# Performance work log

Hardware: AMD Instinct MI355X
Metric: run time of the kernel (lower is better)

Reference implementation:

```python
import jax, jax.numpy as jnp
import numpy as np

V = 50257      # vocab_size
EMB = 300      # emb_size
H = 512        # mcan_flat_out_size (GRU hidden)
HS = 256       # hidden_size (object proposal feature dim)
BH = 256       # bi_hidden_size (encoder output feature dim)
NP = 256       # num_proposal
ML = 50        # max_length (lang seq len)
AL = 20        # answer length -> 19 decode steps
NEG = -1e9


def setup_inputs() -> dict:
    key = jax.random.key(0)
    ks = jax.random.split(key, 30)
    s = 0.02
    n = lambda k, sh: (s * jax.random.normal(k, sh)).astype(jnp.float32)
    d = {}
    d["input_tok"] = jax.random.randint(ks[0], (1,), 0, V, dtype=jnp.int32)
    d["hidden"] = jax.random.normal(ks[1], (1, 1, H), jnp.float32)
    d["encoder_outputs"] = jax.random.normal(ks[2], (ML, BH), jnp.float32)
    d["object_proposals"] = jax.random.normal(ks[3], (NP, HS), jnp.float32)
    d["object_mask"] = jax.random.randint(ks[4], (1, NP), 0, 2, dtype=jnp.int32)
    d["lang_mask"] = jax.random.randint(ks[5], (1, ML), 0, 2, dtype=jnp.int32)
    d["answer_to_vocab"] = jax.random.randint(ks[6], (AL,), 0, V, dtype=jnp.int32)
    # learned params (dropout treated as eval/identity)
    d["emb"] = n(ks[7], (V, EMB))
    cin = H + EMB  # 812
    d["attn_w1"] = n(ks[8], (256, cin)); d["attn_b1"] = jnp.zeros((256,), jnp.float32)
    d["attn_w2"] = n(ks[9], (ML, 256)); d["attn_b2"] = jnp.zeros((ML,), jnp.float32)
    d["attn_op_w1"] = n(ks[10], (256, cin)); d["attn_op_b1"] = jnp.zeros((256,), jnp.float32)
    d["attn_op_w2"] = n(ks[11], (NP, 256)); d["attn_op_b2"] = jnp.zeros((NP,), jnp.float32)
    comb_in = HS + BH + EMB  # 812
    d["cmb_w1"] = n(ks[12], (512, comb_in)); d["cmb_b1"] = jnp.zeros((512,), jnp.float32)
    d["cmb_w2"] = n(ks[13], (H, 512)); d["cmb_b2"] = jnp.zeros((H,), jnp.float32)
    d["gru_w_ih"] = n(ks[14], (3 * H, H)); d["gru_w_hh"] = n(ks[15], (3 * H, H))
    d["gru_b_ih"] = jnp.zeros((3 * H,), jnp.float32); d["gru_b_hh"] = jnp.zeros((3 * H,), jnp.float32)
    d["out_w"] = n(ks[16], (V, H)); d["out_b"] = jnp.zeros((V,), jnp.float32)
    return d


def reference(input_tok, hidden, encoder_outputs, object_proposals, object_mask,
              lang_mask, answer_to_vocab, emb, attn_w1, attn_b1, attn_w2, attn_b2,
              attn_op_w1, attn_op_b1, attn_op_w2, attn_op_b2, cmb_w1, cmb_b1,
              cmb_w2, cmb_b2, gru_w_ih, gru_w_hh, gru_b_ih, gru_b_hh, out_w, out_b):
    obj_m = object_mask.astype(bool)   # [1, NP]
    lang_m = lang_mask.astype(bool)    # [1, ML]
    # teacher forcing: step i embeds answer_to_vocab[i] (step 0 uses input_tok)
    tokens = jnp.concatenate([input_tok, answer_to_vocab[1:-1]])  # [AL-1]

    def step(h, tok):
        # h: [1,1,H]
        x = jax.nn.relu(emb[tok])[None, :]                     # [1,EMB]
        cat = jnp.concatenate([x, h[0]], axis=1)               # [1, EMB+H]
        # object attention
        a_op = jax.nn.relu(cat @ attn_op_w1.T + attn_op_b1) @ attn_op_w2.T + attn_op_b2
        a_op = jax.nn.softmax(jnp.where(obj_m, NEG, a_op), axis=1)   # [1,NP]
        ctx_op = a_op @ object_proposals                       # [1,HS]
        # language attention
        a_l = jax.nn.relu(cat @ attn_w1.T + attn_b1) @ attn_w2.T + attn_b2
        a_l = jax.nn.softmax(jnp.where(lang_m, NEG, a_l), axis=1)    # [1,ML]
        ctx = a_l @ encoder_outputs                            # [1,BH]
        comb = jnp.concatenate([x, ctx, ctx_op], axis=1)       # [1, EMB+BH+HS]
        g = jax.nn.relu(jax.nn.relu(comb @ cmb_w1.T + cmb_b1) @ cmb_w2.T + cmb_b2)  # [1,H]
        # GRU cell (torch gate order: r, z, n)
        gi = g @ gru_w_ih.T + gru_b_ih
        gh = h[0] @ gru_w_hh.T + gru_b_hh
        i_r, i_z, i_n = jnp.split(gi, 3, axis=1)
        h_r, h_z, h_n = jnp.split(gh, 3, axis=1)
        r = jax.nn.sigmoid(i_r + h_r)
        z = jax.nn.sigmoid(i_z + h_z)
        nn_ = jnp.tanh(i_n + r * h_n)
        h_new = (1.0 - z) * nn_ + z * h[0]                     # [1,H]
        logits = h_new @ out_w.T + out_b                       # [1,V]
        return h_new[None], (logits, a_l, a_op)

    _, (logits, attn_w, attn_ob_w) = jax.lax.scan(step, hidden, tokens)
    # logits: [AL-1,1,V]; attn_w: [AL-1,1,ML]; attn_ob_w: [AL-1,1,NP]
    return logits, attn_w, attn_ob_w
```

## Files before the change

### kernel.cpp

```cpp
#include <hip/hip_runtime.h>
#include <math.h>

#define T_STEPS 19
#define V 50257
#define EMB 300
#define HDIM 512
#define NP 256
#define ML 50
#define CIN 812
#define NEGV -1e9f
#define NBLK 64

#define OFF_X      0
#define OFF_POP    5700
#define OFF_PL     10564
#define OFF_PC     15428
#define OFF_HS     25156
#define OFF_H1OP   35396
#define OFF_H1L    35652
#define OFF_C1     37444
#define OFF_G      37956
#define OFF_LOGOP  38468
#define OFF_LOGL   38724
#define OFF_MPROP  38788
#define OFF_MENC   169860
#define OFF_BAR    195460

#define OUT_LOGITS 0
#define OUT_ATTW   ((long)T_STEPS * V)
#define OUT_ATTOB  (OUT_ATTW + (long)T_STEPS * ML)

__device__ __forceinline__ float wred(float v) {
  v += __shfl_xor(v, 32, 64);
  v += __shfl_xor(v, 16, 64);
  v += __shfl_xor(v, 8, 64);
  v += __shfl_xor(v, 4, 64);
  v += __shfl_xor(v, 2, 64);
  v += __shfl_xor(v, 1, 64);
  return v;
}

__device__ __forceinline__ float dot4(float4 a, float4 b) {
  return a.x * b.x + a.y * b.y + a.z * b.z + a.w * b.w;
}

__device__ __forceinline__ void gstore(float* p, float v) {
  __hip_atomic_store(p, v, __ATOMIC_RELAXED, __HIP_MEMORY_SCOPE_AGENT);
}
__device__ __forceinline__ float ld1c(const float* p) {
  return __hip_atomic_load(p, __ATOMIC_RELAXED, __HIP_MEMORY_SCOPE_AGENT);
}
__device__ __forceinline__ float2 ld2c(const float* p) {
  unsigned long long u = __hip_atomic_load((const unsigned long long*)p,
                                           __ATOMIC_RELAXED, __HIP_MEMORY_SCOPE_AGENT);
  float2 r;
  r.x = __uint_as_float((unsigned)u);
  r.y = __uint_as_float((unsigned)(u >> 32));
  return r;
}
__device__ __forceinline__ float4 ld4c(const float* p) {
  float2 a = ld2c(p), b = ld2c(p + 2);
  return make_float4(a.x, a.y, b.x, b.y);
}

__device__ __forceinline__ void gbar(float* wsb, unsigned bar) {
  asm volatile("s_waitcnt vmcnt(0)" ::: "memory");
  __syncthreads();
  unsigned* flags = (unsigned*)(wsb + OFF_BAR) + 16;
  if (threadIdx.x == 0) {
    __hip_atomic_store(flags + 16 * blockIdx.x, bar, __ATOMIC_RELAXED, __HIP_MEMORY_SCOPE_AGENT);
  }
  asm volatile("" ::: "memory");
  if (threadIdx.x < 64) {
    unsigned* f = flags + 16 * threadIdx.x;
    while (__hip_atomic_load(f, __ATOMIC_RELAXED, __HIP_MEMORY_SCOPE_AGENT) < bar) {
      __builtin_amdgcn_s_sleep(1);
    }
  }
  __syncthreads();
}

__global__ void k_pre1(const int* __restrict__ tok0, const int* __restrict__ ans,
                       const float* __restrict__ emb, const float* __restrict__ hidden,
                       float* __restrict__ ws) {
  int tid = blockIdx.x * 256 + threadIdx.x;
  if (tid < T_STEPS * EMB) {
    int s = tid / EMB, j = tid - s * EMB;
    int t = (s == 0) ? tok0[0] : ans[s];
    float v = emb[(long)t * EMB + j];
    ws[OFF_X + tid] = v > 0.f ? v : 0.f;
  } else {
    int k = tid - T_STEPS * EMB;
    if (k < HDIM) ws[OFF_HS + k] = hidden[k];
  }
}

__global__ void k_pre2(const float* __restrict__ w1op, const float* __restrict__ b1op,
                       const float* __restrict__ w1l,  const float* __restrict__ b1l,
                       const float* __restrict__ wc1,  const float* __restrict__ bc1,
                       float* __restrict__ ws) {
  int gw = (blockIdx.x * 256 + threadIdx.x) >> 6;
  int lane = threadIdx.x & 63;
  int s = gw >> 10;
  int rr = gw & 1023;
  if (s >= T_STEPS) return;
  const float* wrow; const float* bias; float* dst; int r;
  if (rr < 256)      { r = rr;       wrow = w1op + (long)r * CIN; bias = b1op; dst = ws + OFF_POP + s * 256 + r; }
  else if (rr < 512) { r = rr - 256; wrow = w1l  + (long)r * CIN; bias = b1l;  dst = ws + OFF_PL  + s * 256 + r; }
  else               { r = rr - 512; wrow = wc1  + (long)r * CIN; bias = bc1;  dst = ws + OFF_PC  + s * 512 + r; }
  const float* x = ws + OFF_X + s * EMB;
  float acc = 0.f;
#pragma unroll
  for (int it = 0; it < 5; ++it) {
    int j = it * 64 + lane;
    if (j < EMB) acc += wrow[j] * x[j];
  }
  acc = wred(acc);
  if (lane == 0) *dst = acc + bias[r];
}

#define LDSF 12850
__global__ void __launch_bounds__(256) k_mprep(const float* __restrict__ cw1,
                                               const float* __restrict__ prop,
                                               const float* __restrict__ enc,
                                               float* __restrict__ ws) {
  __shared__ float lds[LDSF];
  int tid = threadIdx.x, r = blockIdx.x;
  float acc = 0.f;
  for (int kc = 0; kc < 8; ++kc) {
    __syncthreads();
#pragma unroll
    for (int i = 0; i < 8; ++i) {
      int f = tid + 256 * i; int row = f >> 3, q = f & 7;
      float4 v = *(const float4*)(prop + (long)row * 256 + kc * 32 + 4 * q);
      float* p = lds + row * 33 + 4 * q;
      p[0] = v.x; p[1] = v.y; p[2] = v.z; p[3] = v.w;
    }
    __syncthreads();
    const float* wbase = cw1 + (long)r * CIN + 556 + kc * 32;
    const float* pl = lds + tid * 33;
#pragma unroll
    for (int k4 = 0; k4 < 8; ++k4) {
      float4 w4 = *(const float4*)(wbase + 4 * k4);
      const float* pp = pl + 4 * k4;
      acc += w4.x * pp[0] + w4.y * pp[1] + w4.z * pp[2] + w4.w * pp[3];
    }
  }
  ws[OFF_MPROP + (long)r * 256 + tid] = acc;
  __syncthreads();
  for (int i = 0; i < 13; ++i) {
    int f = tid + 256 * i;
    if (f < 3200) {
      int row = f >> 6, q = f & 63;
      float4 v = *(const float4*)(enc + (long)row * 256 + 4 * q);
      float* p = lds + row * 257 + 4 * q;
      p[0] = v.x; p[1] = v.y; p[2] = v.z; p[3] = v.w;
    }
  }
  __syncthreads();
  if (tid < ML) {
    const float* wb2 = cw1 + (long)r * CIN + 300;
    const float* el = lds + tid * 257;
    float a2 = 0.f;
#pragma unroll 8
    for (int k = 0; k < 256; ++k) a2 += wb2[k] * el[k];
    ws[OFF_MENC + (long)r * ML + tid] = a2;
  }
}

__global__ void __launch_bounds__(256) k_recur(
    const float* __restrict__ w1op, const float* __restrict__ w1l,
    const float* __restrict__ whh,  const float* __restrict__ bhh,
    const float* __restrict__ w2op, const float* __restrict__ b2op,
    const float* __restrict__ w2l,  const float* __restrict__ b2l,
    const int* __restrict__ obj_mask, const int* __restrict__ lang_mask,
    const float* __restrict__ wc2,  const float* __restrict__ bc2,
    const float* __restrict__ wih,  const float* __restrict__ bih,
    float* ws, float* __restrict__ out) {
  const int tid = threadIdx.x;
  const int lane = tid & 63;
  const int wv = (blockIdx.x << 2) + (tid >> 6);
  const int r0 = 2 * wv, r1 = 2 * wv + 1;
  unsigned bar = 1;
  __shared__ float red[256];
  __shared__ __align__(16) float sm_aop[256];
  __shared__ float sm_al[64];

  for (int s = 0; s < T_STEPS; ++s) {
    float ghr0, ghz0, ghn0, ghr1, ghz1, ghn1;
    {
      const float* h = ws + OFF_HS + s * HDIM;
      float4 ha = ld4c(h + 4 * lane);
      float4 hb = ld4c(h + 256 + 4 * lane);
      const float* wa0 = (r0 < 256) ? (w1op + (long)r0 * CIN + 300) : (w1l + (long)(r0 - 256) * CIN + 300);
      const float* wa1 = (r1 < 256) ? (w1op + (long)r1 * CIN + 300) : (w1l + (long)(r1 - 256) * CIN + 300);
      float a0 = dot4(*(const float4*)(wa0 + 4 * lane), ha) + dot4(*(const float4*)(wa0 + 256 + 4 * lane), hb);
      float a1 = dot4(*(const float4*)(wa1 + 4 * lane), ha) + dot4(*(const float4*)(wa1 + 256 + 4 * lane), hb);
      const float* p0 = whh + (long)r0 * HDIM;
      const float* p1 = whh + (long)(r0 + 512) * HDIM;
      const float* p2 = whh + (long)(r0 + 1024) * HDIM;
      const float* p3 = whh + (long)r1 * HDIM;
      const float* p4 = whh + (long)(r1 + 512) * HDIM;
      const float* p5 = whh + (long)(r1 + 1024) * HDIM;
      float b0 = dot4(*(const float4*)(p0 + 4 * lane), ha) + dot4(*(const float4*)(p0 + 256 + 4 * lane), hb);
      float b1 = dot4(*(const float4*)(p1 + 4 * lane), ha) + dot4(*(const float4*)(p1 + 256 + 4 * lane), hb);
      float b2 = dot4(*(const float4*)(p2 + 4 * lane), ha) + dot4(*(const float4*)(p2 + 256 + 4 * lane), hb);
      float b3 = dot4(*(const float4*)(p3 + 4 * lane), ha) + dot4(*(const float4*)(p3 + 256 + 4 * lane), hb);
      float b4 = dot4(*(const float4*)(p4 + 4 * lane), ha) + dot4(*(const float4*)(p4 + 256 + 4 * lane), hb);
      float b5 = dot4(*(const float4*)(p5 + 4 * lane), ha) + dot4(*(const float4*)(p5 + 256 + 4 * lane), hb);
      a0 = wred(a0); a1 = wred(a1);
      b0 = wred(b0); b1 = wred(b1); b2 = wred(b2);
      b3 = wred(b3); b4 = wred(b4); b5 = wred(b5);
      ghr0 = b0 + bhh[r0]; ghz0 = b1 + bhh[512 + r0]; ghn0 = b2 + bhh[1024 + r0];
      ghr1 = b3 + bhh[r1]; ghz1 = b4 + bhh[512 + r1]; ghn1 = b5 + bhh[1024 + r1];
      if (lane == 0) {
        float v0 = a0 + ((r0 < 256) ? ws[OFF_POP + s * 256 + r0] : ws[OFF_PL + s * 256 + (r0 - 256)]);
        float v1 = a1 + ((r1 < 256) ? ws[OFF_POP + s * 256 + r1] : ws[OFF_PL + s * 256 + (r1 - 256)]);
        float* d0 = (r0 < 256) ? (ws + OFF_H1OP + r0) : (ws + OFF_H1L + (r0 - 256));
        float* d1 = (r1 < 256) ? (ws + OFF_H1OP + r1) : (ws + OFF_H1L + (r1 - 256));
        gstore(d0, v0 > 0.f ? v0 : 0.f);
        gstore(d1, v1 > 0.f ? v1 : 0.f);
      }
    }
    gbar(ws, bar++);
    {
      float4 h1 = ld4c(ws + OFF_H1OP + 4 * lane);
      const float* wr = w2op + (long)wv * 256;
      float acc = wred(dot4(*(const float4*)(wr + 4 * lane), h1));
      if (lane == 0) gstore(ws + OFF_LOGOP + wv, acc + b2op[wv]);
      if (wv < ML) {
        float4 h1l = ld4c(ws + OFF_H1L + 4 * lane);
        const float* wrl = w2l + (long)wv * 256;
        float accl = wred(dot4(*(const float4*)(wrl + 4 * lane), h1l));
        if (lane == 0) gstore(ws + OFF_LOGL + wv, accl + b2l[wv]);
      }
    }
    gbar(ws, bar++);
    {
      float lv = ld1c(ws + OFF_LOGOP + tid);
      float vo = (obj_mask[tid] != 0) ? NEGV : lv;
      red[tid] = vo; __syncthreads();
      for (int st = 128; st > 0; st >>= 1) { if (tid < st) red[tid] = fmaxf(red[tid], red[tid + st]); __syncthreads(); }
      float mo = red[0]; __syncthreads();
      float eo = expf(vo - mo);
      red[tid] = eo; __syncthreads();
      for (int st = 128; st > 0; st >>= 1) { if (tid < st) red[tid] += red[tid + st]; __syncthreads(); }
      float aop = eo / red[0];
      sm_aop[tid] = aop;
      __syncthreads();
      float ll = (tid < ML) ? ld1c(ws + OFF_LOGL + tid) : 0.f;
      float vl = (tid < ML) ? ((lang_mask[tid] != 0) ? NEGV : ll) : -3e38f;
      red[tid] = vl; __syncthreads();
      for (int st = 128; st > 0; st >>= 1) { if (tid < st) red[tid] = fmaxf(red[tid], red[tid + st]); __syncthreads(); }
      float ml_ = red[0]; __syncthreads();
      float el = (tid < ML) ? expf(vl - ml_) : 0.f;
      red[tid] = el; __syncthreads();
      for (int st = 128; st > 0; st >>= 1) { if (tid < st) red[tid] += red[tid + st]; __syncthreads(); }
      float al = el / red[0];
      if (tid < 64) sm_al[tid] = (tid < ML) ? al : 0.f;
      __syncthreads();
      if (blockIdx.x == 0) {
        out[OUT_ATTOB + (long)s * NP + tid] = aop;
        if (tid < ML) out[OUT_ATTW + (long)s * ML + tid] = al;
      }
      float4 a4 = *(const float4*)(&sm_aop[4 * lane]);
      const float* mp0 = ws + OFF_MPROP + (long)r0 * 256;
      const float* mp1 = ws + OFF_MPROP + (long)r1 * 256;
      float acc0 = dot4(*(const float4*)(mp0 + 4 * lane), a4);
      float acc1 = dot4(*(const float4*)(mp1 + 4 * lane), a4);
      if (lane < ML) {
        float alv = sm_al[lane];
        acc0 += ws[OFF_MENC + (long)r0 * ML + lane] * alv;
        acc1 += ws[OFF_MENC + (long)r1 * ML + lane] * alv;
      }
      acc0 = wred(acc0); acc1 = wred(acc1);
      if (lane == 0) {
        float v0 = acc0 + ws[OFF_PC + s * HDIM + r0];
        float v1 = acc1 + ws[OFF_PC + s * HDIM + r1];
        gstore(ws + OFF_C1 + r0, v0 > 0.f ? v0 : 0.f);
        gstore(ws + OFF_C1 + r1, v1 > 0.f ? v1 : 0.f);
      }
    }
    gbar(ws, bar++);
    {
      float4 ca = ld4c(ws + OFF_C1 + 4 * lane);
      float4 cb = ld4c(ws + OFF_C1 + 256 + 4 * lane);
      const float* q0 = wc2 + (long)r0 * HDIM;
      const float* q1 = wc2 + (long)r1 * HDIM;
      float acc0 = dot4(*(const float4*)(q0 + 4 * lane), ca) + dot4(*(const float4*)(q0 + 256 + 4 * lane), cb);
      float acc1 = dot4(*(const float4*)(q1 + 4 * lane), ca) + dot4(*(const float4*)(q1 + 256 + 4 * lane), cb);
      acc0 = wred(acc0); acc1 = wred(acc1);
      if (lane == 0) {
        float v0 = acc0 + bc2[r0];
        float v1 = acc1 + bc2[r1];
        gstore(ws + OFF_G + r0, v0 > 0.f ? v0 : 0.f);
        gstore(ws + OFF_G + r1, v1 > 0.f ? v1 : 0.f);
      }
    }
    gbar(ws, bar++);
    {
      float4 ga = ld4c(ws + OFF_G + 4 * lane);
      float4 gb = ld4c(ws + OFF_G + 256 + 4 * lane);
      const float* p0 = wih + (long)r0 * HDIM;
      const float* p1 = wih + (long)(r0 + 512) * HDIM;
      const float* p2 = wih + (long)(r0 + 1024) * HDIM;
      const float* p3 = wih + (long)r1 * HDIM;
      const float* p4 = wih + (long)(r1 + 512) * HDIM;
      const float* p5 = wih + (long)(r1 + 1024) * HDIM;
      float a0 = dot4(*(const float4*)(p0 + 4 * lane), ga) + dot4(*(const float4*)(p0 + 256 + 4 * lane), gb);
      float a1 = dot4(*(const float4*)(p1 + 4 * lane), ga) + dot4(*(const float4*)(p1 + 256 + 4 * lane), gb);
      float a2 = dot4(*(const float4*)(p2 + 4 * lane), ga) + dot4(*(const float4*)(p2 + 256 + 4 * lane), gb);
      float a3 = dot4(*(const float4*)(p3 + 4 * lane), ga) + dot4(*(const float4*)(p3 + 256 + 4 * lane), gb);
      float a4_ = dot4(*(const float4*)(p4 + 4 * lane), ga) + dot4(*(const float4*)(p4 + 256 + 4 * lane), gb);
      float a5 = dot4(*(const float4*)(p5 + 4 * lane), ga) + dot4(*(const float4*)(p5 + 256 + 4 * lane), gb);
      a0 = wred(a0); a1 = wred(a1); a2 = wred(a2);
      a3 = wred(a3); a4_ = wred(a4_); a5 = wred(a5);
      if (lane == 0) {
        float ir0 = a0 + bih[r0], iz0 = a1 + bih[512 + r0], in0 = a2 + bih[1024 + r0];
        float rg0 = 1.f / (1.f + expf(-(ir0 + ghr0)));
        float zg0 = 1.f / (1.f + expf(-(iz0 + ghz0)));
        float ng0 = tanhf(in0 + rg0 * ghn0);
        float hp0 = ld1c(ws + OFF_HS + s * HDIM + r0);
        gstore(ws + OFF_HS + (s + 1) * HDIM + r0, (1.f - zg0) * ng0 + zg0 * hp0);
        float ir1 = a3 + bih[r1], iz1 = a4_ + bih[512 + r1], in1 = a5 + bih[1024 + r1];
        float rg1 = 1.f / (1.f + expf(-(ir1 + ghr1)));
        float zg1 = 1.f / (1.f + expf(-(iz1 + ghz1)));
        float ng1 = tanhf(in1 + rg1 * ghn1);
        float hp1 = ld1c(ws + OFF_HS + s * HDIM + r1);
        gstore(ws + OFF_HS + (s + 1) * HDIM + r1, (1.f - zg1) * ng1 + zg1 * hp1);
      }
    }
    gbar(ws, bar++);
  }
}

__global__ void __launch_bounds__(256) k_final2(const float* __restrict__ ow,
                                                const float* __restrict__ ob,
                                                const float* __restrict__ ws,
                                                float* __restrict__ out) {
  __shared__ __align__(16) float wl[256 * 36];
  __shared__ __align__(16) float hl[T_STEPS * 512];
  int tid = threadIdx.x;
  long rbase = (long)blockIdx.x * 256;
  for (int i = tid; i < T_STEPS * 512; i += 256) hl[i] = ws[OFF_HS + 512 + i];
  float4 st[8];
#pragma unroll
  for (int i = 0; i < 8; ++i) {
    int f = tid + 256 * i; int row = f >> 3, q = f & 7;
    long r = rbase + row;
    st[i] = (r < V) ? *(const float4*)(ow + r * 512 + 4 * q) : make_float4(0.f, 0.f, 0.f, 0.f);
  }
  float acc[T_STEPS];
#pragma unroll
  for (int s = 0; s < T_STEPS; ++s) acc[s] = 0.f;
  __syncthreads();
  for (int c = 0; c < 16; ++c) {
#pragma unroll
    for (int i = 0; i < 8; ++i) {
      int f = tid + 256 * i; int row = f >> 3, q = f & 7;
      float* p = wl + row * 36 + 4 * q;
      p[0] = st[i].x; p[1] = st[i].y; p[2] = st[i].z; p[3] = st[i].w;
    }
    __syncthreads();
    if (c < 15) {
#pragma unroll
      for (int i = 0; i < 8; ++i) {
        int f = tid + 256 * i; int row = f >> 3, q = f & 7;
        long r = rbase + row;
        st[i] = (r < V) ? *(const float4*)(ow + r * 512 + (c + 1) * 32 + 4 * q) : make_float4(0.f, 0.f, 0.f, 0.f);
      }
    }
    const float* wp = wl + tid * 36;
#pragma unroll
    for (int kq = 0; kq < 8; ++kq) {
      float4 w4 = *(const float4*)(wp + 4 * kq);
      const float* hb = hl + c * 32 + 4 * kq;
#pragma unroll
      for (int s = 0; s < T_STEPS; ++s) {
        float4 h4 = *(const float4*)(hb + s * 512);
        acc[s] += dot4(w4, h4);
      }
    }
    __syncthreads();
  }
  long r = rbase + tid;
  if (r < V) {
    float b = ob[r];
#pragma unroll
    for (int s = 0; s < T_STEPS; ++s) out[OUT_LOGITS + (long)s * V + r] = acc[s] + b;
  }
}

extern "C" void kernel_launch(void* const* d_in, const int* in_sizes, int n_in,
                              void* d_out, int out_size, void* d_ws, size_t ws_size,
                              hipStream_t stream) {
  const int*   input_tok  = (const int*)d_in[0];
  const float* hidden     = (const float*)d_in[1];
  const float* enc        = (const float*)d_in[2];
  const float* prop       = (const float*)d_in[3];
  const int*   obj_mask   = (const int*)d_in[4];
  const int*   lang_mask  = (const int*)d_in[5];
  const int*   ans        = (const int*)d_in[6];
  const float* emb        = (const float*)d_in[7];
  const float* attn_w1    = (const float*)d_in[8];
  const float* attn_b1    = (const float*)d_in[9];
  const float* attn_w2    = (const float*)d_in[10];
  const float* attn_b2    = (const float*)d_in[11];
  const float* attn_op_w1 = (const float*)d_in[12];
  const float* attn_op_b1 = (const float*)d_in[13];
  const float* attn_op_w2 = (const float*)d_in[14];
  const float* attn_op_b2 = (const float*)d_in[15];
  const float* cmb_w1     = (const float*)d_in[16];
  const float* cmb_b1     = (const float*)d_in[17];
  const float* cmb_w2     = (const float*)d_in[18];
  const float* cmb_b2     = (const float*)d_in[19];
  const float* gw_ih      = (const float*)d_in[20];
  const float* gw_hh      = (const float*)d_in[21];
  const float* gb_ih      = (const float*)d_in[22];
  const float* gb_hh      = (const float*)d_in[23];
  const float* out_w      = (const float*)d_in[24];
  const float* out_b      = (const float*)d_in[25];
  float* out = (float*)d_out;
  float* ws  = (float*)d_ws;

  hipMemsetAsync((char*)d_ws + (size_t)OFF_BAR * 4, 0, 8448, stream);
  k_pre1<<<25, 256, 0, stream>>>(input_tok, ans, emb, hidden, ws);
  k_pre2<<<4864, 256, 0, stream>>>(attn_op_w1, attn_op_b1, attn_w1, attn_b1, cmb_w1, cmb_b1, ws);
  k_mprep<<<512, 256, 0, stream>>>(cmb_w1, prop, enc, ws);
  k_recur<<<NBLK, 256, 0, stream>>>(attn_op_w1, attn_w1, gw_hh, gb_hh,
                                    attn_op_w2, attn_op_b2, attn_w2, attn_b2,
                                    obj_mask, lang_mask, cmb_w2, cmb_b2,
                                    gw_ih, gb_ih, ws, out);
  k_final2<<<(V + 255) / 256, 256, 0, stream>>>(out_w, out_b, ws, out);
}
```

Baseline: 419.2 us.

## Keep recurrent weights in registers across steps and transpose final LDS tile

The persistent recurrent kernel now loads every weight slice it needs (attention W1 hidden part, GRU W_hh/W_ih, combine W2, attention W2, precomputed proposal and encoder projections, biases) into registers once before the step loop, instead of re-reading them from global memory or cache in each of the 19 steps. It sets launch bounds to one block per CU to allow the higher register count. The output-projection kernel changes its LDS weight tile to a transposed layout with float4 stores, to cut bank conflicts and scalar stores. Workspace offsets and the barrier memset size are also compacted.

```diff
diff --git a/kernel.cpp b/kernel.cpp
--- a/kernel.cpp
+++ b/kernel.cpp
@@ -18,13 +18,13 @@
 #define OFF_HS     25156
 #define OFF_H1OP   35396
 #define OFF_H1L    35652
-#define OFF_C1     37444
-#define OFF_G      37956
-#define OFF_LOGOP  38468
-#define OFF_LOGL   38724
-#define OFF_MPROP  38788
-#define OFF_MENC   169860
-#define OFF_BAR    195460
+#define OFF_C1     35908
+#define OFF_G      36420
+#define OFF_LOGOP  36932
+#define OFF_LOGL   37188
+#define OFF_MPROP  37252
+#define OFF_MENC   168324
+#define OFF_BAR    193924
 
 #define OUT_LOGITS 0
 #define OUT_ATTW   ((long)T_STEPS * V)
@@ -168,7 +168,7 @@
   }
 }
 
-__global__ void __launch_bounds__(256) k_recur(
+__global__ void __launch_bounds__(256, 1) k_recur(
     const float* __restrict__ w1op, const float* __restrict__ w1l,
     const float* __restrict__ whh,  const float* __restrict__ bhh,
     const float* __restrict__ w2op, const float* __restrict__ b2op,
@@ -181,38 +181,64 @@
   const int lane = tid & 63;
   const int wv = (blockIdx.x << 2) + (tid >> 6);
   const int r0 = 2 * wv, r1 = 2 * wv + 1;
+  const int l4 = 4 * lane;
   unsigned bar = 1;
   __shared__ float red[256];
   __shared__ __align__(16) float sm_aop[256];
   __shared__ float sm_al[64];
 
+  const float* wa0p = (r0 < 256) ? (w1op + (long)r0 * CIN + 300) : (w1l + (long)(r0 - 256) * CIN + 300);
+  const float* wa1p = (r1 < 256) ? (w1op + (long)r1 * CIN + 300) : (w1l + (long)(r1 - 256) * CIN + 300);
+  float4 WA00 = *(const float4*)(wa0p + l4), WA01 = *(const float4*)(wa0p + 256 + l4);
+  float4 WA10 = *(const float4*)(wa1p + l4), WA11 = *(const float4*)(wa1p + 256 + l4);
+  const float* q;
+  q = whh + (long)r0 * HDIM;           float4 WH00 = *(const float4*)(q + l4), WH01 = *(const float4*)(q + 256 + l4);
+  q = whh + (long)(r0 + 512) * HDIM;   float4 WH10 = *(const float4*)(q + l4), WH11 = *(const float4*)(q + 256 + l4);
+  q = whh + (long)(r0 + 1024) * HDIM;  float4 WH20 = *(const float4*)(q + l4), WH21 = *(const float4*)(q + 256 + l4);
+  q = whh + (long)r1 * HDIM;           float4 WH30 = *(const float4*)(q + l4), WH31 = *(const float4*)(q + 256 + l4);
+  q = whh + (long)(r1 + 512) * HDIM;   float4 WH40 = *(const float4*)(q + l4), WH41 = *(const float4*)(q + 256 + l4);
+  q = whh + (long)(r1 + 1024) * HDIM;  float4 WH50 = *(const float4*)(q + l4), WH51 = *(const float4*)(q + 256 + l4);
+  float4 W2  = *(const float4*)(w2op + (long)wv * 256 + l4);
+  float4 W2L = (wv < ML) ? *(const float4*)(w2l + (long)wv * 256 + l4) : make_float4(0.f, 0.f, 0.f, 0.f);
+  float4 MP0 = *(const float4*)(ws + OFF_MPROP + (long)r0 * 256 + l4);
+  float4 MP1 = *(const float4*)(ws + OFF_MPROP + (long)r1 * 256 + l4);
+  float  ME0 = (lane < ML) ? ws[OFF_MENC + (long)r0 * ML + lane] : 0.f;
+  float  ME1 = (lane < ML) ? ws[OFF_MENC + (long)r1 * ML + lane] : 0.f;
+  q = wc2 + (long)r0 * HDIM;           float4 WC00 = *(const float4*)(q + l4), WC01 = *(const float4*)(q + 256 + l4);
+  q = wc2 + (long)r1 * HDIM;           float4 WC10 = *(const float4*)(q + l4), WC11 = *(const float4*)(q + 256 + l4);
+  q = wih + (long)r0 * HDIM;           float4 WI00 = *(const float4*)(q + l4), WI01 = *(const float4*)(q + 256 + l4);
+  q = wih + (long)(r0 + 512) * HDIM;   float4 WI10 = *(const float4*)(q + l4), WI11 = *(const float4*)(q + 256 + l4);
+  q = wih + (long)(r0 + 1024) * HDIM;  float4 WI20 = *(const float4*)(q + l4), WI21 = *(const float4*)(q + 256 + l4);
+  q = wih + (long)r1 * HDIM;           float4 WI30 = *(const float4*)(q + l4), WI31 = *(const float4*)(q + 256 + l4);
+  q = wih + (long)(r1 + 512) * HDIM;   float4 WI40 = *(const float4*)(q + l4), WI41 = *(const float4*)(q + 256 + l4);
+  q = wih + (long)(r1 + 1024) * HDIM;  float4 WI50 = *(const float4*)(q + l4), WI51 = *(const float4*)(q + 256 + l4);
+  float BH0 = bhh[r0], BH1 = bhh[512 + r0], BH2 = bhh[1024 + r0];
+  float BH3 = bhh[r1], BH4 = bhh[512 + r1], BH5 = bhh[1024 + r1];
+  float BI0 = bih[r0], BI1 = bih[512 + r0], BI2 = bih[1024 + r0];
+  float BI3 = bih[r1], BI4 = bih[512 + r1], BI5 = bih[1024 + r1];
+  float BC0 = bc2[r0], BC1 = bc2[r1];
+  float B2  = b2op[wv];
+  float B2Lv = (wv < ML) ? b2l[wv] : 0.f;
+
   for (int s = 0; s < T_STEPS; ++s) {
     float ghr0, ghz0, ghn0, ghr1, ghz1, ghn1;
     {
       const float* h = ws + OFF_HS + s * HDIM;
-      float4 ha = ld4c(h + 4 * lane);
-      float4 hb = ld4c(h + 256 + 4 * lane);
-      const float* wa0 = (r0 < 256) ? (w1op + (long)r0 * CIN + 300) : (w1l + (long)(r0 - 256) * CIN + 300);
-      const float* wa1 = (r1 < 256) ? (w1op + (long)r1 * CIN + 300) : (w1l + (long)(r1 - 256) * CIN + 300);
-      float a0 = dot4(*(const float4*)(wa0 + 4 * lane), ha) + dot4(*(const float4*)(wa0 + 256 + 4 * lane), hb);
-      float a1 = dot4(*(const float4*)(wa1 + 4 * lane), ha) + dot4(*(const float4*)(wa1 + 256 + 4 * lane), hb);
-      const float* p0 = whh + (long)r0 * HDIM;
-      const float* p1 = whh + (long)(r0 + 512) * HDIM;
-      const float* p2 = whh + (long)(r0 + 1024) * HDIM;
-      const float* p3 = whh + (long)r1 * HDIM;
-      const float* p4 = whh + (long)(r1 + 512) * HDIM;
-      const float* p5 = whh + (long)(r1 + 1024) * HDIM;
-      float b0 = dot4(*(const float4*)(p0 + 4 * lane), ha) + dot4(*(const float4*)(p0 + 256 + 4 * lane), hb);
-      float b1 = dot4(*(const float4*)(p1 + 4 * lane), ha) + dot4(*(const float4*)(p1 + 256 + 4 * lane), hb);
-      float b2 = dot4(*(const float4*)(p2 + 4 * lane), ha) + dot4(*(const float4*)(p2 + 256 + 4 * lane), hb);
-      float b3 = dot4(*(const float4*)(p3 + 4 * lane), ha) + dot4(*(const float4*)(p3 + 256 + 4 * lane), hb);
-      float b4 = dot4(*(const float4*)(p4 + 4 * lane), ha) + dot4(*(const float4*)(p4 + 256 + 4 * lane), hb);
-      float b5 = dot4(*(const float4*)(p5 + 4 * lane), ha) + dot4(*(const float4*)(p5 + 256 + 4 * lane), hb);
+      float4 ha = ld4c(h + l4);
+      float4 hb = ld4c(h + 256 + l4);
+      float a0 = dot4(WA00, ha) + dot4(WA01, hb);
+      float a1 = dot4(WA10, ha) + dot4(WA11, hb);
+      float b0 = dot4(WH00, ha) + dot4(WH01, hb);
+      float b1 = dot4(WH10, ha) + dot4(WH11, hb);
+      float b2 = dot4(WH20, ha) + dot4(WH21, hb);
+      float b3 = dot4(WH30, ha) + dot4(WH31, hb);
+      float b4 = dot4(WH40, ha) + dot4(WH41, hb);
+      float b5 = dot4(WH50, ha) + dot4(WH51, hb);
       a0 = wred(a0); a1 = wred(a1);
       b0 = wred(b0); b1 = wred(b1); b2 = wred(b2);
       b3 = wred(b3); b4 = wred(b4); b5 = wred(b5);
-      ghr0 = b0 + bhh[r0]; ghz0 = b1 + bhh[512 + r0]; ghn0 = b2 + bhh[1024 + r0];
-      ghr1 = b3 + bhh[r1]; ghz1 = b4 + bhh[512 + r1]; ghn1 = b5 + bhh[1024 + r1];
+      ghr0 = b0 + BH0; ghz0 = b1 + BH1; ghn0 = b2 + BH2;
+      ghr1 = b3 + BH3; ghz1 = b4 + BH4; ghn1 = b5 + BH5;
       if (lane == 0) {
         float v0 = a0 + ((r0 < 256) ? ws[OFF_POP + s * 256 + r0] : ws[OFF_PL + s * 256 + (r0 - 256)]);
         float v1 = a1 + ((r1 < 256) ? ws[OFF_POP + s * 256 + r1] : ws[OFF_PL + s * 256 + (r1 - 256)]);
@@ -224,15 +250,13 @@
     }
     gbar(ws, bar++);
     {
-      float4 h1 = ld4c(ws + OFF_H1OP + 4 * lane);
-      const float* wr = w2op + (long)wv * 256;
-      float acc = wred(dot4(*(const float4*)(wr + 4 * lane), h1));
-      if (lane == 0) gstore(ws + OFF_LOGOP + wv, acc + b2op[wv]);
+      float4 h1 = ld4c(ws + OFF_H1OP + l4);
+      float acc = wred(dot4(W2, h1));
+      if (lane == 0) gstore(ws + OFF_LOGOP + wv, acc + B2);
       if (wv < ML) {
-        float4 h1l = ld4c(ws + OFF_H1L + 4 * lane);
-        const float* wrl = w2l + (long)wv * 256;
-        float accl = wred(dot4(*(const float4*)(wrl + 4 * lane), h1l));
-        if (lane == 0) gstore(ws + OFF_LOGL + wv, accl + b2l[wv]);
+        float4 h1l = ld4c(ws + OFF_H1L + l4);
+        float accl = wred(dot4(W2L, h1l));
+        if (lane == 0) gstore(ws + OFF_LOGL + wv, accl + B2Lv);
       }
     }
     gbar(ws, bar++);
@@ -248,7 +272,8 @@
       float aop = eo / red[0];
       sm_aop[tid] = aop;
       __syncthreads();
-      float ll = (tid < ML) ? ld1c(ws + OFF_LOGL + tid) : 0.f;
+      float ll = 0.f;
+      if (tid < ML) ll = ld1c(ws + OFF_LOGL + tid);
       float vl = (tid < ML) ? ((lang_mask[tid] != 0) ? NEGV : ll) : -3e38f;
       red[tid] = vl; __syncthreads();
       for (int st = 128; st > 0; st >>= 1) { if (tid < st) red[tid] = fmaxf(red[tid], red[tid + st]); __syncthreads(); }
@@ -263,15 +288,13 @@
         out[OUT_ATTOB + (long)s * NP + tid] = aop;
         if (tid < ML) out[OUT_ATTW + (long)s * ML + tid] = al;
       }
-      float4 a4 = *(const float4*)(&sm_aop[4 * lane]);
-      const float* mp0 = ws + OFF_MPROP + (long)r0 * 256;
-      const float* mp1 = ws + OFF_MPROP + (long)r1 * 256;
-      float acc0 = dot4(*(const float4*)(mp0 + 4 * lane), a4);
-      float acc1 = dot4(*(const float4*)(mp1 + 4 * lane), a4);
+      float4 a4 = *(const float4*)(&sm_aop[l4]);
+      float acc0 = dot4(MP0, a4);
+      float acc1 = dot4(MP1, a4);
       if (lane < ML) {
         float alv = sm_al[lane];
-        acc0 += ws[OFF_MENC + (long)r0 * ML + lane] * alv;
-        acc1 += ws[OFF_MENC + (long)r1 * ML + lane] * alv;
+        acc0 += ME0 * alv;
+        acc1 += ME1 * alv;
       }
       acc0 = wred(acc0); acc1 = wred(acc1);
       if (lane == 0) {
@@ -283,46 +306,38 @@
     }
     gbar(ws, bar++);
     {
-      float4 ca = ld4c(ws + OFF_C1 + 4 * lane);
-      float4 cb = ld4c(ws + OFF_C1 + 256 + 4 * lane);
-      const float* q0 = wc2 + (long)r0 * HDIM;
-      const float* q1 = wc2 + (long)r1 * HDIM;
-      float acc0 = dot4(*(const float4*)(q0 + 4 * lane), ca) + dot4(*(const float4*)(q0 + 256 + 4 * lane), cb);
-      float acc1 = dot4(*(const float4*)(q1 + 4 * lane), ca) + dot4(*(const float4*)(q1 + 256 + 4 * lane), cb);
+      float4 ca = ld4c(ws + OFF_C1 + l4);
+      float4 cb = ld4c(ws + OFF_C1 + 256 + l4);
+      float acc0 = dot4(WC00, ca) + dot4(WC01, cb);
+      float acc1 = dot4(WC10, ca) + dot4(WC11, cb);
       acc0 = wred(acc0); acc1 = wred(acc1);
       if (lane == 0) {
-        float v0 = acc0 + bc2[r0];
-        float v1 = acc1 + bc2[r1];
+        float v0 = acc0 + BC0;
+        float v1 = acc1 + BC1;
         gstore(ws + OFF_G + r0, v0 > 0.f ? v0 : 0.f);
         gstore(ws + OFF_G + r1, v1 > 0.f ? v1 : 0.f);
       }
     }
     gbar(ws, bar++);
     {
-      float4 ga = ld4c(ws + OFF_G + 4 * lane);
-      float4 gb = ld4c(ws + OFF_G + 256 + 4 * lane);
-      const float* p0 = wih + (long)r0 * HDIM;
-      const float* p1 = wih + (long)(r0 + 512) * HDIM;
-      const float* p2 = wih + (long)(r0 + 1024) * HDIM;
-      const float* p3 = wih + (long)r1 * HDIM;
-      const float* p4 = wih + (long)(r1 + 512) * HDIM;
-      const float* p5 = wih + (long)(r1 + 1024) * HDIM;
-      float a0 = dot4(*(const float4*)(p0 + 4 * lane), ga) + dot4(*(const float4*)(p0 + 256 + 4 * lane), gb);
-      float a1 = dot4(*(const float4*)(p1 + 4 * lane), ga) + dot4(*(const float4*)(p1 + 256 + 4 * lane), gb);
-      float a2 = dot4(*(const float4*)(p2 + 4 * lane), ga) + dot4(*(const float4*)(p2 + 256 + 4 * lane), gb);
-      float a3 = dot4(*(const float4*)(p3 + 4 * lane), ga) + dot4(*(const float4*)(p3 + 256 + 4 * lane), gb);
-      float a4_ = dot4(*(const float4*)(p4 + 4 * lane), ga) + dot4(*(const float4*)(p4 + 256 + 4 * lane), gb);
-      float a5 = dot4(*(const float4*)(p5 + 4 * lane), ga) + dot4(*(const float4*)(p5 + 256 + 4 * lane), gb);
+      float4 ga = ld4c(ws + OFF_G + l4);
+      float4 gb = ld4c(ws + OFF_G + 256 + l4);
+      float a0 = dot4(WI00, ga) + dot4(WI01, gb);
+      float a1 = dot4(WI10, ga) + dot4(WI11, gb);
+      float a2 = dot4(WI20, ga) + dot4(WI21, gb);
+      float a3 = dot4(WI30, ga) + dot4(WI31, gb);
+      float a4_ = dot4(WI40, ga) + dot4(WI41, gb);
+      float a5 = dot4(WI50, ga) + dot4(WI51, gb);
       a0 = wred(a0); a1 = wred(a1); a2 = wred(a2);
       a3 = wred(a3); a4_ = wred(a4_); a5 = wred(a5);
       if (lane == 0) {
-        float ir0 = a0 + bih[r0], iz0 = a1 + bih[512 + r0], in0 = a2 + bih[1024 + r0];
+        float ir0 = a0 + BI0, iz0 = a1 + BI1, in0 = a2 + BI2;
         float rg0 = 1.f / (1.f + expf(-(ir0 + ghr0)));
         float zg0 = 1.f / (1.f + expf(-(iz0 + ghz0)));
         float ng0 = tanhf(in0 + rg0 * ghn0);
         float hp0 = ld1c(ws + OFF_HS + s * HDIM + r0);
         gstore(ws + OFF_HS + (s + 1) * HDIM + r0, (1.f - zg0) * ng0 + zg0 * hp0);
-        float ir1 = a3 + bih[r1], iz1 = a4_ + bih[512 + r1], in1 = a5 + bih[1024 + r1];
+        float ir1 = a3 + BI3, iz1 = a4_ + BI4, in1 = a5 + BI5;
         float rg1 = 1.f / (1.f + expf(-(ir1 + ghr1)));
         float zg1 = 1.f / (1.f + expf(-(iz1 + ghz1)));
         float ng1 = tanhf(in1 + rg1 * ghn1);
@@ -334,11 +349,12 @@
   }
 }
 
+#define WL(row, q) ((q) * 1032 + 4 * (row))
 __global__ void __launch_bounds__(256) k_final2(const float* __restrict__ ow,
                                                 const float* __restrict__ ob,
                                                 const float* __restrict__ ws,
                                                 float* __restrict__ out) {
-  __shared__ __align__(16) float wl[256 * 36];
+  __shared__ __align__(16) float wl[8 * 1032];
   __shared__ __align__(16) float hl[T_STEPS * 512];
   int tid = threadIdx.x;
   long rbase = (long)blockIdx.x * 256;
@@ -358,8 +374,7 @@
 #pragma unroll
     for (int i = 0; i < 8; ++i) {
       int f = tid + 256 * i; int row = f >> 3, q = f & 7;
-      float* p = wl + row * 36 + 4 * q;
-      p[0] = st[i].x; p[1] = st[i].y; p[2] = st[i].z; p[3] = st[i].w;
+      *(float4*)(&wl[WL(row, q)]) = st[i];
     }
     __syncthreads();
     if (c < 15) {
@@ -370,10 +385,9 @@
         st[i] = (r < V) ? *(const float4*)(ow + r * 512 + (c + 1) * 32 + 4 * q) : make_float4(0.f, 0.f, 0.f, 0.f);
       }
     }
-    const float* wp = wl + tid * 36;
 #pragma unroll
     for (int kq = 0; kq < 8; ++kq) {
-      float4 w4 = *(const float4*)(wp + 4 * kq);
+      float4 w4 = *(const float4*)(&wl[WL(tid, kq)]);
       const float* hb = hl + c * 32 + 4 * kq;
 #pragma unroll
       for (int s = 0; s < T_STEPS; ++s) {
@@ -423,7 +437,7 @@
   float* out = (float*)d_out;
   float* ws  = (float*)d_ws;
 
-  hipMemsetAsync((char*)d_ws + (size_t)OFF_BAR * 4, 0, 8448, stream);
+  hipMemsetAsync((char*)d_ws + (size_t)OFF_BAR * 4, 0, 4608, stream);
   k_pre1<<<25, 256, 0, stream>>>(input_tok, ans, emb, hidden, ws);
   k_pre2<<<4864, 256, 0, stream>>>(attn_op_w1, attn_op_b1, attn_w1, attn_b1, cmb_w1, cmb_b1, ws);
   k_mprep<<<512, 256, 0, stream>>>(cmb_w1, prop, enc, ws);
```

Result: no change. 412.4 us (-1.6%).
